# Kernel tuning notes

Hardware: AMD Instinct MI355X
Metric: run time of the kernel (lower is better)

The kernel has to match this reference:

```python
import jax, jax.numpy as jnp
import numpy as np

NGRAPH = 200   # batched graphs
NPG = 100      # nodes per graph
N = NGRAPH * NPG
EPG = 800      # edges per graph
E = NGRAPH * EPG
IN_DIM = 21
HID = 256      # nodes (hidden width)
NHEAD = 1
NLAYER = 4
EPS = 1e-5
SLOPE = 0.2    # GATv2 leaky_relu negative slope


def _edge_softmax(score, dst):
    # score: [E, H]; softmax over incoming edges of each dst node
    m = jax.ops.segment_max(score, dst, num_segments=N)
    m = jnp.where(jnp.isfinite(m), m, 0.0)
    ex = jnp.exp(score - m[dst])
    den = jax.ops.segment_sum(ex, dst, num_segments=N)
    return ex / den[dst]


def _gat(h, src, dst, Ws, bs, Wd, bd, a, res):
    # GATv2Conv: share_weights=False, residual, allow_zero_in_degree
    Hh, Dd = a.shape
    fs = (h @ Ws + bs).reshape(N, Hh, Dd)
    fd = (h @ Wd + bd).reshape(N, Hh, Dd)
    e = jax.nn.leaky_relu(fs[src] + fd[dst], SLOPE)          # [E,H,D]
    score = jnp.einsum('ehd,hd->eh', e, a)                    # [E,H]
    alpha = _edge_softmax(score, dst)                         # [E,H]
    rst = jax.ops.segment_sum(alpha[:, :, None] * fs[src], dst, num_segments=N)
    return (rst + res.reshape(N, Hh, Dd)).reshape(N, Hh * Dd), alpha


def _bn(x, g, b):
    # BatchNorm1d, training-mode batch stats (biased var), affine
    mu = x.mean(0)
    var = x.var(0)
    return g * (x - mu) / jnp.sqrt(var + EPS) + b


def _graph_mean(h, gid):
    s = jax.ops.segment_sum(h, gid, num_segments=NGRAPH)
    cnt = jax.ops.segment_sum(jnp.ones((h.shape[0], 1), h.dtype), gid, num_segments=NGRAPH)
    return s / cnt


def _forward(x, Ws0, bs0, Wd0, bd0, a0, Wres0, g0, be0,
             Ws_r, bs_r, Wd_r, bd_r, a_r, g_r, be_r,
             fc1_W, fc1_b, gfc, bfc, fc2_W, fc2_b, src, dst, gid):
    feats, attns = [], []
    h, al = _gat(x, src, dst, Ws0, bs0, Wd0, bd0, a0, x @ Wres0)
    h = jax.nn.relu(_bn(h, g0, be0))
    feats.append(_graph_mean(h, gid)); attns.append(al[:, 0])
    for l in range(NLAYER - 1):
        h2, al = _gat(h, src, dst, Ws_r[l], bs_r[l], Wd_r[l], bd_r[l], a_r[l], h)
        h = jax.nn.relu(_bn(h2, g_r[l], be_r[l]))
        feats.append(_graph_mean(h, gid)); attns.append(al[:, 0])
    feat = jnp.concatenate(feats, axis=1)                     # [B, NLAYER*HID]
    feat = jax.nn.relu(_bn(feat @ fc1_W + fc1_b, gfc, bfc))   # dropout is identity (eval)
    feat = feat @ fc2_W + fc2_b                               # [B, 5]
    attns = jnp.stack(attns).T                                # [E, NLAYER]
    return feat, attns


def setup_inputs() -> dict:
    key = jax.random.key(0)
    ks = jax.random.split(key, 24)
    sc = 0.05
    eoff = jnp.repeat(jnp.arange(NGRAPH, dtype=jnp.int32) * NPG, EPG)
    src = jax.random.randint(ks[0], (E,), 0, NPG, dtype=jnp.int32) + eoff
    dst = jax.random.randint(ks[1], (E,), 0, NPG, dtype=jnp.int32) + eoff
    gid = jnp.repeat(jnp.arange(NGRAPH, dtype=jnp.int32), NPG)
    return {
        'x': jax.random.normal(ks[2], (N, IN_DIM), jnp.float32),
        'Ws0': jax.random.normal(ks[3], (IN_DIM, HID), jnp.float32) * sc,
        'bs0': jnp.zeros((HID,), jnp.float32),
        'Wd0': jax.random.normal(ks[4], (IN_DIM, HID), jnp.float32) * sc,
        'bd0': jnp.zeros((HID,), jnp.float32),
        'a0': jax.random.normal(ks[5], (NHEAD, HID // NHEAD), jnp.float32) * sc,
        'Wres0': jax.random.normal(ks[6], (IN_DIM, HID), jnp.float32) * sc,
        'g0': jnp.ones((HID,), jnp.float32),
        'be0': jnp.zeros((HID,), jnp.float32),
        'Ws_r': jax.random.normal(ks[7], (NLAYER - 1, HID, HID), jnp.float32) * sc,
        'bs_r': jnp.zeros((NLAYER - 1, HID), jnp.float32),
        'Wd_r': jax.random.normal(ks[8], (NLAYER - 1, HID, HID), jnp.float32) * sc,
        'bd_r': jnp.zeros((NLAYER - 1, HID), jnp.float32),
        'a_r': jax.random.normal(ks[9], (NLAYER - 1, NHEAD, HID // NHEAD), jnp.float32) * sc,
        'g_r': jnp.ones((NLAYER - 1, HID), jnp.float32),
        'be_r': jnp.zeros((NLAYER - 1, HID), jnp.float32),
        'fc1_W': jax.random.normal(ks[10], (NLAYER * HID, HID), jnp.float32) * sc,
        'fc1_b': jnp.zeros((HID,), jnp.float32),
        'gfc': jnp.ones((HID,), jnp.float32),
        'bfc': jnp.zeros((HID,), jnp.float32),
        'fc2_W': jax.random.normal(ks[11], (HID, 5), jnp.float32) * sc,
        'fc2_b': jnp.zeros((5,), jnp.float32),
        'src': src, 'dst': dst, 'gid': gid,
    }


def reference(x, Ws0, bs0, Wd0, bd0, a0, Wres0, g0, be0,
              Ws_r, bs_r, Wd_r, bd_r, a_r, g_r, be_r,
              fc1_W, fc1_b, gfc, bfc, fc2_W, fc2_b, src, dst, gid):
    return _forward(x, Ws0, bs0, Wd0, bd0, a0, Wres0, g0, be0,
                    Ws_r, bs_r, Wd_r, bd_r, a_r, g_r, be_r,
                    fc1_W, fc1_b, gfc, bfc, fc2_W, fc2_b, src, dst, gid)
```

## Files before the change

### kernel.cpp

```cpp
#include <hip/hip_runtime.h>

typedef __bf16 bf16x8 __attribute__((ext_vector_type(8)));
typedef __bf16 bf16x4 __attribute__((ext_vector_type(4)));
typedef float f32x4 __attribute__((ext_vector_type(4)));

constexpr int cN   = 20000;
constexpr int cG   = 200;
constexpr int cNPG = 100;
constexpr int cE   = 160000;
constexpr int cEPG = 800;
constexpr int cHID = 256;
constexpr int cIN  = 21;
constexpr float cEPS   = 1e-5f;
constexpr float cSLOPE = 0.2f;
constexpr int cCH  = 32;
constexpr int cCHS = 25;
constexpr int cPART = 32;

__device__ __forceinline__ float4 cvt4(bf16x4 v) {
    return make_float4((float)v.x, (float)v.y, (float)v.z, (float)v.w);
}
__device__ __forceinline__ bf16x4 tobf4(float4 v) {
    bf16x4 r;
    r.x = (__bf16)v.x; r.y = (__bf16)v.y; r.z = (__bf16)v.z; r.w = (__bf16)v.w;
    return r;
}

__device__ __forceinline__ void gl_lds16(const __bf16* g, __bf16* l) {
    __builtin_amdgcn_global_load_lds(
        (const __attribute__((address_space(1))) void*)g,
        (__attribute__((address_space(3))) void*)l, 16, 0, 0);
}

__global__ __launch_bounds__(256) void k_in_gemm(
    const float* __restrict__ x,
    const float* __restrict__ Ws, const float* __restrict__ bs,
    const float* __restrict__ Wd, const float* __restrict__ bd,
    const float* __restrict__ Wr,
    __bf16* __restrict__ fsb, __bf16* __restrict__ fdb, __bf16* __restrict__ resb,
    float* __restrict__ bnz)
{
    __shared__ float xl[8 * cIN];
    int tid = threadIdx.x;
    if (blockIdx.x == 0)
        for (int i = tid; i < 2 * cPART * cHID; i += 256) bnz[i] = 0.f;
    int rb  = blockIdx.x * 8;
    if (tid < 8 * cIN) xl[tid] = x[(size_t)rb * cIN + tid];
    __syncthreads();
    int j = tid;
    float ws[cIN], wd[cIN], wr[cIN];
#pragma unroll
    for (int k = 0; k < cIN; ++k) {
        ws[k] = Ws[k * cHID + j];
        wd[k] = Wd[k * cHID + j];
        wr[k] = Wr[k * cHID + j];
    }
    float vbs = bs[j], vbd = bd[j];
    for (int r = 0; r < 8; ++r) {
        float as = vbs, ad = vbd, ar = 0.f;
#pragma unroll
        for (int k = 0; k < cIN; ++k) {
            float xv = xl[r * cIN + k];
            as += xv * ws[k];
            ad += xv * wd[k];
            ar += xv * wr[k];
        }
        size_t o = (size_t)(rb + r) * cHID + j;
        fsb[o] = (__bf16)as; fdb[o] = (__bf16)ad; resb[o] = (__bf16)ar;
    }
}

__global__ __launch_bounds__(256) void k_wcvt(
    const float* __restrict__ Ws_r, const float* __restrict__ Wd_r,
    __bf16* __restrict__ WT)
{
    int mat = blockIdx.y;
    int l = mat >> 1;
    const float* W = ((mat & 1) ? Wd_r : Ws_r) + (size_t)l * cHID * cHID;
    __bf16* T = WT + (size_t)l * 512 * cHID + (size_t)(mat & 1) * cHID * cHID;
    int k = blockIdx.x, n = threadIdx.x;
    T[(size_t)n * cHID + k] = (__bf16)W[(size_t)k * cHID + n];
}

__global__ __launch_bounds__(256) void k_gemm_mfma(
    const __bf16* __restrict__ hb, const __bf16* __restrict__ Wcat,
    const float* __restrict__ bs, const float* __restrict__ bd,
    __bf16* __restrict__ fsb, __bf16* __restrict__ fdb,
    float* __restrict__ bnz)
{
    __shared__ __bf16 lA[128 * 32];
    __shared__ __bf16 lB[128 * 32];
    int tid = threadIdx.x, lane = tid & 63, w = tid >> 6;
    if (blockIdx.x == 0 && blockIdx.y == 0)
        for (int i = tid; i < 2 * cPART * cHID; i += 256) bnz[i] = 0.f;
    int wr = w >> 1, wc = w & 1;
    int rc = lane & 15, kg = lane >> 4;
    int m0  = blockIdx.x * 128;
    int bn0 = blockIdx.y * 128;

    f32x4 acc[4][4];
#pragma unroll
    for (int m = 0; m < 4; ++m)
#pragma unroll
        for (int n = 0; n < 4; ++n)
            acc[m][n] = (f32x4){0.f, 0.f, 0.f, 0.f};

#pragma unroll 1
    for (int ks = 0; ks < 8; ++ks) {
        int k0 = ks * 32;
#pragma unroll
        for (int j = 0; j < 2; ++j) {
            int c   = j * 256 + tid;
            int row = c >> 2, ci = c & 3;
            __bf16* dA = &lA[(size_t)(j * 256 + w * 64) * 8];
            __bf16* dB = &lB[(size_t)(j * 256 + w * 64) * 8];
            gl_lds16(hb   + (size_t)(m0  + row) * cHID + k0 + ci * 8, dA);
            gl_lds16(Wcat + (size_t)(bn0 + row) * cHID + k0 + ci * 8, dB);
        }
        __syncthreads();

        bf16x8 a[4], b[4];
#pragma unroll
        for (int m = 0; m < 4; ++m)
            a[m] = *(const bf16x8*)&lA[(wr * 64 + m * 16 + rc) * 32 + kg * 8];
#pragma unroll
        for (int n = 0; n < 4; ++n)
            b[n] = *(const bf16x8*)&lB[(wc * 64 + n * 16 + rc) * 32 + kg * 8];
#pragma unroll
        for (int m = 0; m < 4; ++m)
#pragma unroll
            for (int n = 0; n < 4; ++n)
                acc[m][n] = __builtin_amdgcn_mfma_f32_16x16x32_bf16(a[m], b[n], acc[m][n], 0, 0, 0);
        __syncthreads();
    }

#pragma unroll
    for (int m = 0; m < 4; ++m) {
        int rbase = m0 + wr * 64 + m * 16 + kg * 4;
#pragma unroll
        for (int n = 0; n < 4; ++n) {
            int col = bn0 + wc * 64 + n * 16 + rc;
            bool isS = col < cHID;
            int  cc  = isS ? col : col - cHID;
            float bias = isS ? bs[cc] : bd[cc];
            __bf16* dst = isS ? fsb : fdb;
#pragma unroll
            for (int i = 0; i < 4; ++i) {
                int r = rbase + i;
                if (r < cN)
                    dst[(size_t)r * cHID + cc] = (__bf16)(acc[m][n][i] + bias);
            }
        }
    }
}

__global__ __launch_bounds__(256) void k_csr(
    const int* __restrict__ dst, int* __restrict__ csr,
    int* __restrict__ off, int* __restrict__ deg)
{
    __shared__ int dstl[cEPG];
    __shared__ int cnt[cCH * 128];
    __shared__ int offl[cNPG];
    __shared__ int tot[128];
    int g = blockIdx.x, tid = threadIdx.x;
    int nb = g * cNPG, eb = g * cEPG;

    for (int i = tid; i < cEPG; i += 256) dstl[i] = dst[eb + i] - nb;
    for (int i = tid; i < cCH * 128; i += 256) cnt[i] = 0;
    __syncthreads();

    for (int i = tid; i < cEPG; i += 256)
        atomicAdd(&cnt[(i / cCHS) * 128 + dstl[i]], 1);
    __syncthreads();

    int mytot = 0;
    if (tid < cNPG) {
        int run = 0;
        for (int c = 0; c < cCH; ++c) {
            int t = cnt[c * 128 + tid];
            cnt[c * 128 + tid] = run;
            run += t;
        }
        mytot = run;
    }
    if (tid < 128) tot[tid] = (tid < cNPG) ? mytot : 0;
    __syncthreads();
    for (int ofs = 1; ofs < 128; ofs <<= 1) {
        int t = 0;
        if (tid < 128 && tid >= ofs) t = tot[tid - ofs];
        __syncthreads();
        if (tid < 128) tot[tid] += t;
        __syncthreads();
    }
    if (tid < cNPG) {
        int excl = tot[tid] - mytot;
        offl[tid] = excl;
        off[nb + tid] = eb + excl;
        deg[nb + tid] = mytot;
    }
    __syncthreads();

    if (tid < cCH) {
        for (int j = 0; j < cCHS; ++j) {
            int i = tid * cCHS + j;
            int n = dstl[i];
            int k = cnt[tid * 128 + n]++;
            csr[eb + offl[n] + k] = eb + i;
        }
    }
}

__global__ __launch_bounds__(256) void k_edge2(
    const __bf16* __restrict__ fsb, const __bf16* __restrict__ fdb,
    const __bf16* __restrict__ resb, const float* __restrict__ avec,
    const int* __restrict__ csr, const int* __restrict__ off,
    const int* __restrict__ deg, const int* __restrict__ src,
    __bf16* __restrict__ hpb, float* __restrict__ attn_out,
    float* __restrict__ spill, float* __restrict__ psum,
    float* __restrict__ pssq, float* __restrict__ fcl)
{
    __shared__ int   sidx[4][64];
    __shared__ int   eidx[4][64];
    __shared__ float exbuf[4][64];
    __shared__ float hblk[4][256];
    int tid = threadIdx.x, lane = tid & 63, w = tid >> 6;
    int bid = blockIdx.x;
    if (bid < cG)
        fcl[(size_t)bid * (4 * cHID) + tid] = 0.f;
    int g   = bid % cG;
    int nid = g * cNPG + (bid / cG) * 4 + w;
    int dg = deg[nid], base = off[nid];

    for (int i = lane; i < dg && i < 64; i += 64) {
        int e = csr[base + i];
        eidx[w][i] = e;
        sidx[w][i] = src[e];
    }

    float4 a4  = *(const float4*)(avec + lane * 4);
    float4 fd4 = cvt4(*(const bf16x4*)(fdb + (size_t)nid * cHID + lane * 4));
    float4 r4  = cvt4(*(const bf16x4*)(resb + (size_t)nid * cHID + lane * 4));
    const __bf16* fsl = fsb + lane * 4;

    bf16x4 fA{}, fB{};
    if (dg > 0) fA = *(const bf16x4*)(fsl + (size_t)sidx[w][0] * cHID);
    if (dg > 1) fB = *(const bf16x4*)(fsl + (size_t)sidx[w][1] * cHID);

    float den = 0.f;
    float4 acc = {0.f, 0.f, 0.f, 0.f};
    for (int i = 0; i < dg; ++i) {
        float4 f4 = cvt4(fA);
        fA = fB;
        if (i + 2 < dg) {
            int s2 = (i + 2 < 64) ? sidx[w][i + 2] : src[csr[base + i + 2]];
            fB = *(const bf16x4*)(fsl + (size_t)s2 * cHID);
        }
        float v0 = f4.x + fd4.x, v1 = f4.y + fd4.y;
        float v2 = f4.z + fd4.z, v3 = f4.w + fd4.w;
        v0 = v0 > 0.f ? v0 : cSLOPE * v0;
        v1 = v1 > 0.f ? v1 : cSLOPE * v1;
        v2 = v2 > 0.f ? v2 : cSLOPE * v2;
        v3 = v3 > 0.f ? v3 : cSLOPE * v3;
        float part = v0 * a4.x + v1 * a4.y + v2 * a4.z + v3 * a4.w;
#pragma unroll
        for (int o = 32; o; o >>= 1) part += __shfl_xor(part, o);
        float ex = __expf(part);
        den += ex;
        acc.x += ex * f4.x; acc.y += ex * f4.y;
        acc.z += ex * f4.z; acc.w += ex * f4.w;
        if (lane == 0) {
            if (i < 64) exbuf[w][i] = ex;
            else        spill[csr[base + i]] = ex;
        }
    }
    float inv = (dg > 0) ? 1.f / den : 0.f;

    for (int i = lane; i < dg; i += 64) {
        float ex = (i < 64) ? exbuf[w][i] : spill[csr[base + i]];
        int e    = (i < 64) ? eidx[w][i]  : csr[base + i];
        attn_out[(size_t)e * 4] = ex * inv;
    }

    float4 o4 = {acc.x * inv + r4.x, acc.y * inv + r4.y,
                 acc.z * inv + r4.z, acc.w * inv + r4.w};
    *(bf16x4*)(hpb + (size_t)nid * cHID + lane * 4) = tobf4(o4);
    *(float4*)&hblk[w][lane * 4] = o4;
    __syncthreads();

    float v0 = hblk[0][tid], v1 = hblk[1][tid], v2 = hblk[2][tid], v3 = hblk[3][tid];
    int slot = (bid & (cPART - 1)) * cHID + tid;
    atomicAdd(&psum[slot], v0 + v1 + v2 + v3);
    atomicAdd(&pssq[slot], v0 * v0 + v1 * v1 + v2 * v2 + v3 * v3);
}

__global__ __launch_bounds__(256) void k_bn_apply(
    const __bf16* __restrict__ hpb,
    const float* __restrict__ psum, const float* __restrict__ pssq,
    const float* __restrict__ gamma, const float* __restrict__ beta,
    __bf16* __restrict__ hb, float* __restrict__ featcat_l)
{
    int j = threadIdx.x, g = blockIdx.x, q = blockIdx.y;
    float s = 0.f, qq = 0.f;
#pragma unroll
    for (int k = 0; k < cPART; ++k) {
        s  += psum[k * cHID + j];
        qq += pssq[k * cHID + j];
    }
    float mu  = s * (1.f / cN);
    float var = qq * (1.f / cN) - mu * mu;
    float sc  = gamma[j] * rsqrtf(var + cEPS);
    float sh  = beta[j] - mu * sc;
    float fsum = 0.f;
    int r0 = g * cNPG + q * 25;
    for (int r = 0; r < 25; ++r) {
        size_t i = (size_t)(r0 + r) * cHID + j;
        float v = (float)hpb[i] * sc + sh;
        v = v > 0.f ? v : 0.f;
        hb[i] = (__bf16)v;
        fsum += v;
    }
    atomicAdd(&featcat_l[(size_t)g * (4 * cHID) + j], fsum * (1.f / cNPG));
}

__global__ __launch_bounds__(256) void k_fc1(
    const float* __restrict__ featcat, const float* __restrict__ W,
    const float* __restrict__ b, float* __restrict__ out)
{
    __shared__ float row[4 * cHID];
    int g = blockIdx.x, j = threadIdx.x;
    for (int i = j; i < 4 * cHID; i += 256) row[i] = featcat[(size_t)g * (4 * cHID) + i];
    __syncthreads();
    float acc = b[j];
    for (int k = 0; k < 4 * cHID; ++k) acc += row[k] * W[(size_t)k * cHID + j];
    out[(size_t)g * cHID + j] = acc;
}

__global__ __launch_bounds__(256) void k_fc_bn(
    float* __restrict__ f2, const float* __restrict__ gamma, const float* __restrict__ beta)
{
    int j = threadIdx.x;
    float s = 0.f, q = 0.f;
    for (int r = 0; r < cG; ++r) { float v = f2[(size_t)r * cHID + j]; s += v; q += v * v; }
    float mu  = s * (1.f / cG);
    float var = q * (1.f / cG) - mu * mu;
    float sc  = gamma[j] * rsqrtf(var + cEPS);
    float sh  = beta[j] - mu * sc;
    for (int r = 0; r < cG; ++r) {
        float v = f2[(size_t)r * cHID + j] * sc + sh;
        f2[(size_t)r * cHID + j] = v > 0.f ? v : 0.f;
    }
}

__global__ __launch_bounds__(256) void k_fc2(
    const float* __restrict__ f2, const float* __restrict__ W,
    const float* __restrict__ b, float* __restrict__ out)
{
    int t = blockIdx.x * 256 + threadIdx.x;
    if (t >= cG * 5) return;
    int r = t / 5, o = t % 5;
    float acc = b[o];
    for (int k = 0; k < cHID; ++k) acc += f2[(size_t)r * cHID + k] * W[k * 5 + o];
    out[t] = acc;
}

extern "C" void kernel_launch(void* const* d_in, const int* in_sizes, int n_in,
                              void* d_out, int out_size, void* d_ws, size_t ws_size,
                              hipStream_t stream)
{
    (void)in_sizes; (void)n_in; (void)out_size; (void)ws_size;
    const float* x     = (const float*)d_in[0];
    const float* Ws0   = (const float*)d_in[1];
    const float* bs0   = (const float*)d_in[2];
    const float* Wd0   = (const float*)d_in[3];
    const float* bd0   = (const float*)d_in[4];
    const float* a0    = (const float*)d_in[5];
    const float* Wres0 = (const float*)d_in[6];
    const float* g0    = (const float*)d_in[7];
    const float* be0   = (const float*)d_in[8];
    const float* Ws_r  = (const float*)d_in[9];
    const float* bs_r  = (const float*)d_in[10];
    const float* Wd_r  = (const float*)d_in[11];
    const float* bd_r  = (const float*)d_in[12];
    const float* a_r   = (const float*)d_in[13];
    const float* g_r   = (const float*)d_in[14];
    const float* be_r  = (const float*)d_in[15];
    const float* fc1_W = (const float*)d_in[16];
    const float* fc1_b = (const float*)d_in[17];
    const float* gfc   = (const float*)d_in[18];
    const float* bfc   = (const float*)d_in[19];
    const float* fc2_W = (const float*)d_in[20];
    const float* fc2_b = (const float*)d_in[21];
    const int*   src   = (const int*)d_in[22];
    const int*   dst   = (const int*)d_in[23];
    float* out = (float*)d_out;

    char* p = (char*)d_ws;
    float* featcat = (float*)p; p += (size_t)cG * 4 * cHID * 4;
    float* feat2   = (float*)p; p += (size_t)cG * cHID * 4;
    float* psum    = (float*)p; p += (size_t)cPART * cHID * 4;
    float* pssq    = (float*)p; p += (size_t)cPART * cHID * 4;
    float* spill   = (float*)p; p += (size_t)cE * 4;
    int*   csr     = (int*)p;   p += (size_t)cE * 4;
    int*   offv    = (int*)p;   p += (size_t)cN * 4;
    int*   degv    = (int*)p;   p += (size_t)cN * 4;
    __bf16* hpb    = (__bf16*)p; p += (size_t)cN * cHID * 2;
    __bf16* hb     = (__bf16*)p; p += (size_t)cN * cHID * 2;
    __bf16* resb0  = (__bf16*)p; p += (size_t)cN * cHID * 2;
    __bf16* fsb    = (__bf16*)p; p += (size_t)cN * cHID * 2;
    __bf16* fdb    = (__bf16*)p; p += (size_t)cN * cHID * 2;
    __bf16* WT     = (__bf16*)p; p += (size_t)3 * 512 * cHID * 2;

    k_wcvt<<<dim3(cHID, 6), 256, 0, stream>>>(Ws_r, Wd_r, WT);
    k_csr<<<cG, 256, 0, stream>>>(dst, csr, offv, degv);

    k_in_gemm<<<cN / 8, 256, 0, stream>>>(x, Ws0, bs0, Wd0, bd0, Wres0,
                                          fsb, fdb, resb0, psum);

    for (int l = 0; l < 4; ++l) {
        if (l > 0) {
            k_gemm_mfma<<<dim3(157, 4), 256, 0, stream>>>(
                hb,
                WT + (size_t)(l - 1) * 512 * cHID,
                bs_r + (size_t)(l - 1) * cHID, bd_r + (size_t)(l - 1) * cHID,
                fsb, fdb, psum);
        }
        const float* ap = (l == 0) ? a0 : a_r + (size_t)(l - 1) * cHID;
        const __bf16* rb = (l == 0) ? resb0 : hb;
        float* fcl = featcat + (size_t)l * cHID;
        k_edge2<<<cN / 4, 256, 0, stream>>>(fsb, fdb, rb, ap, csr, offv, degv, src,
                                            hpb, out + 1000 + l, spill,
                                            psum, pssq, fcl);
        const float* gm = (l == 0) ? g0  : g_r  + (size_t)(l - 1) * cHID;
        const float* bt = (l == 0) ? be0 : be_r + (size_t)(l - 1) * cHID;
        k_bn_apply<<<dim3(cG, 4), 256, 0, stream>>>(hpb, psum, pssq, gm, bt, hb, fcl);
    }

    k_fc1<<<cG, 256, 0, stream>>>(featcat, fc1_W, fc1_b, feat2);
    k_fc_bn<<<1, 256, 0, stream>>>(feat2, gfc, bfc);
    k_fc2<<<4, 256, 0, stream>>>(feat2, fc2_W, fc2_b, out);
}
```

Before: 289.4 us.

## Merge setup kernels, deepen edge gather prefetch, skip final-layer h write

Folds the weight-transpose and CSR-build kernels into one launch, with different block ranges doing each job. The edge kernel's source-feature prefetch goes from two edges ahead to four, to hide more gather latency. The last layer's BN-apply no longer writes the normalized node features, since only the graph means are used afterwards. The deeper prefetch costs extra registers per lane.

```diff
diff --git a/kernel.cpp b/kernel.cpp
--- a/kernel.cpp
+++ b/kernel.cpp
@@ -70,16 +70,72 @@
     }
 }
 
-__global__ __launch_bounds__(256) void k_wcvt(
+__global__ __launch_bounds__(256) void k_setup(
     const float* __restrict__ Ws_r, const float* __restrict__ Wd_r,
-    __bf16* __restrict__ WT)
-{
-    int mat = blockIdx.y;
-    int l = mat >> 1;
-    const float* W = ((mat & 1) ? Wd_r : Ws_r) + (size_t)l * cHID * cHID;
-    __bf16* T = WT + (size_t)l * 512 * cHID + (size_t)(mat & 1) * cHID * cHID;
-    int k = blockIdx.x, n = threadIdx.x;
-    T[(size_t)n * cHID + k] = (__bf16)W[(size_t)k * cHID + n];
+    __bf16* __restrict__ WT,
+    const int* __restrict__ dst, int* __restrict__ csr,
+    int* __restrict__ off, int* __restrict__ deg)
+{
+    int bid = blockIdx.x, tid = threadIdx.x;
+    if (bid < 6 * cHID) {
+        int mat = bid >> 8;
+        int k   = bid & 255;
+        int l = mat >> 1;
+        const float* W = ((mat & 1) ? Wd_r : Ws_r) + (size_t)l * cHID * cHID;
+        __bf16* T = WT + (size_t)l * 512 * cHID + (size_t)(mat & 1) * cHID * cHID;
+        T[(size_t)tid * cHID + k] = (__bf16)W[(size_t)k * cHID + tid];
+        return;
+    }
+    __shared__ int dstl[cEPG];
+    __shared__ int cnt[cCH * 128];
+    __shared__ int offl[cNPG];
+    __shared__ int tot[128];
+    int g = bid - 6 * cHID;
+    int nb = g * cNPG, eb = g * cEPG;
+
+    for (int i = tid; i < cEPG; i += 256) dstl[i] = dst[eb + i] - nb;
+    for (int i = tid; i < cCH * 128; i += 256) cnt[i] = 0;
+    __syncthreads();
+
+    for (int i = tid; i < cEPG; i += 256)
+        atomicAdd(&cnt[(i / cCHS) * 128 + dstl[i]], 1);
+    __syncthreads();
+
+    int mytot = 0;
+    if (tid < cNPG) {
+        int run = 0;
+        for (int c = 0; c < cCH; ++c) {
+            int t = cnt[c * 128 + tid];
+            cnt[c * 128 + tid] = run;
+            run += t;
+        }
+        mytot = run;
+    }
+    if (tid < 128) tot[tid] = (tid < cNPG) ? mytot : 0;
+    __syncthreads();
+    for (int ofs = 1; ofs < 128; ofs <<= 1) {
+        int t = 0;
+        if (tid < 128 && tid >= ofs) t = tot[tid - ofs];
+        __syncthreads();
+        if (tid < 128) tot[tid] += t;
+        __syncthreads();
+    }
+    if (tid < cNPG) {
+        int excl = tot[tid] - mytot;
+        offl[tid] = excl;
+        off[nb + tid] = eb + excl;
+        deg[nb + tid] = mytot;
+    }
+    __syncthreads();
+
+    if (tid < cCH) {
+        for (int j = 0; j < cCHS; ++j) {
+            int i = tid * cCHS + j;
+            int n = dstl[i];
+            int k = cnt[tid * 128 + n]++;
+            csr[eb + offl[n] + k] = eb + i;
+        }
+    }
 }
 
 __global__ __launch_bounds__(256) void k_gemm_mfma(
@@ -150,62 +206,6 @@
                 if (r < cN)
                     dst[(size_t)r * cHID + cc] = (__bf16)(acc[m][n][i] + bias);
             }
-        }
-    }
-}
-
-__global__ __launch_bounds__(256) void k_csr(
-    const int* __restrict__ dst, int* __restrict__ csr,
-    int* __restrict__ off, int* __restrict__ deg)
-{
-    __shared__ int dstl[cEPG];
-    __shared__ int cnt[cCH * 128];
-    __shared__ int offl[cNPG];
-    __shared__ int tot[128];
-    int g = blockIdx.x, tid = threadIdx.x;
-    int nb = g * cNPG, eb = g * cEPG;
-
-    for (int i = tid; i < cEPG; i += 256) dstl[i] = dst[eb + i] - nb;
-    for (int i = tid; i < cCH * 128; i += 256) cnt[i] = 0;
-    __syncthreads();
-
-    for (int i = tid; i < cEPG; i += 256)
-        atomicAdd(&cnt[(i / cCHS) * 128 + dstl[i]], 1);
-    __syncthreads();
-
-    int mytot = 0;
-    if (tid < cNPG) {
-        int run = 0;
-        for (int c = 0; c < cCH; ++c) {
-            int t = cnt[c * 128 + tid];
-            cnt[c * 128 + tid] = run;
-            run += t;
-        }
-        mytot = run;
-    }
-    if (tid < 128) tot[tid] = (tid < cNPG) ? mytot : 0;
-    __syncthreads();
-    for (int ofs = 1; ofs < 128; ofs <<= 1) {
-        int t = 0;
-        if (tid < 128 && tid >= ofs) t = tot[tid - ofs];
-        __syncthreads();
-        if (tid < 128) tot[tid] += t;
-        __syncthreads();
-    }
-    if (tid < cNPG) {
-        int excl = tot[tid] - mytot;
-        offl[tid] = excl;
-        off[nb + tid] = eb + excl;
-        deg[nb + tid] = mytot;
-    }
-    __syncthreads();
-
-    if (tid < cCH) {
-        for (int j = 0; j < cCHS; ++j) {
-            int i = tid * cCHS + j;
-            int n = dstl[i];
-            int k = cnt[tid * 128 + n]++;
-            csr[eb + offl[n] + k] = eb + i;
         }
     }
 }
@@ -242,18 +242,20 @@
     float4 r4  = cvt4(*(const bf16x4*)(resb + (size_t)nid * cHID + lane * 4));
     const __bf16* fsl = fsb + lane * 4;
 
-    bf16x4 fA{}, fB{};
-    if (dg > 0) fA = *(const bf16x4*)(fsl + (size_t)sidx[w][0] * cHID);
-    if (dg > 1) fB = *(const bf16x4*)(fsl + (size_t)sidx[w][1] * cHID);
+    bf16x4 f0{}, f1{}, f2{}, f3{};
+    if (dg > 0) f0 = *(const bf16x4*)(fsl + (size_t)sidx[w][0] * cHID);
+    if (dg > 1) f1 = *(const bf16x4*)(fsl + (size_t)sidx[w][1] * cHID);
+    if (dg > 2) f2 = *(const bf16x4*)(fsl + (size_t)sidx[w][2] * cHID);
+    if (dg > 3) f3 = *(const bf16x4*)(fsl + (size_t)sidx[w][3] * cHID);
 
     float den = 0.f;
     float4 acc = {0.f, 0.f, 0.f, 0.f};
     for (int i = 0; i < dg; ++i) {
-        float4 f4 = cvt4(fA);
-        fA = fB;
-        if (i + 2 < dg) {
-            int s2 = (i + 2 < 64) ? sidx[w][i + 2] : src[csr[base + i + 2]];
-            fB = *(const bf16x4*)(fsl + (size_t)s2 * cHID);
+        float4 f4 = cvt4(f0);
+        f0 = f1; f1 = f2; f2 = f3;
+        if (i + 4 < dg) {
+            int s4 = (i + 4 < 64) ? sidx[w][i + 4] : src[csr[base + i + 4]];
+            f3 = *(const bf16x4*)(fsl + (size_t)s4 * cHID);
         }
         float v0 = f4.x + fd4.x, v1 = f4.y + fd4.y;
         float v2 = f4.z + fd4.z, v3 = f4.w + fd4.w;
@@ -297,7 +299,7 @@
     const __bf16* __restrict__ hpb,
     const float* __restrict__ psum, const float* __restrict__ pssq,
     const float* __restrict__ gamma, const float* __restrict__ beta,
-    __bf16* __restrict__ hb, float* __restrict__ featcat_l)
+    __bf16* __restrict__ hb, float* __restrict__ featcat_l, int writeH)
 {
     int j = threadIdx.x, g = blockIdx.x, q = blockIdx.y;
     float s = 0.f, qq = 0.f;
@@ -316,7 +318,7 @@
         size_t i = (size_t)(r0 + r) * cHID + j;
         float v = (float)hpb[i] * sc + sh;
         v = v > 0.f ? v : 0.f;
-        hb[i] = (__bf16)v;
+        if (writeH) hb[i] = (__bf16)v;
         fsum += v;
     }
     atomicAdd(&featcat_l[(size_t)g * (4 * cHID) + j], fsum * (1.f / cNPG));
@@ -410,8 +412,7 @@
     __bf16* fdb    = (__bf16*)p; p += (size_t)cN * cHID * 2;
     __bf16* WT     = (__bf16*)p; p += (size_t)3 * 512 * cHID * 2;
 
-    k_wcvt<<<dim3(cHID, 6), 256, 0, stream>>>(Ws_r, Wd_r, WT);
-    k_csr<<<cG, 256, 0, stream>>>(dst, csr, offv, degv);
+    k_setup<<<6 * cHID + cG, 256, 0, stream>>>(Ws_r, Wd_r, WT, dst, csr, offv, degv);
 
     k_in_gemm<<<cN / 8, 256, 0, stream>>>(x, Ws0, bs0, Wd0, bd0, Wres0,
                                           fsb, fdb, resb0, psum);
@@ -432,7 +433,8 @@
                                             psum, pssq, fcl);
         const float* gm = (l == 0) ? g0  : g_r  + (size_t)(l - 1) * cHID;
         const float* bt = (l == 0) ? be0 : be_r + (size_t)(l - 1) * cHID;
-        k_bn_apply<<<dim3(cG, 4), 256, 0, stream>>>(hpb, psum, pssq, gm, bt, hb, fcl);
+        k_bn_apply<<<dim3(cG, 4), 256, 0, stream>>>(hpb, psum, pssq, gm, bt, hb, fcl,
+                                                    l < 3 ? 1 : 0);
     }
 
     k_fc1<<<cG, 256, 0, stream>>>(featcat, fc1_W, fc1_b, feat2);
```

Result: slower. 310.5 us (+7.3%).
